# Kernel optimization log

Hardware: AMD Instinct MI355X
Metric: run time of the kernel (lower is better)

Reference implementation:

```python
import jax, jax.numpy as jnp
import numpy as np

E = 1280   # embed_dim
H = 16     # num_heads
D = E // H # head_dim = 80
S = 3072   # total tokens


def _rotate_half(x):
    x1, x2 = x[..., : D // 2], x[..., D // 2:]
    return jnp.concatenate((-x2, x1), axis=-1)


def setup_inputs() -> dict:
    key = jax.random.key(0)
    ks = jax.random.split(key, 7)
    x = jax.random.normal(ks[0], (S, E), dtype=jnp.float32)
    # rotary embeddings: cos/sin of random angles, shape (S, head_dim)
    ang = jax.random.uniform(ks[1], (S, D), dtype=jnp.float32) * (2 * np.pi)
    cos = jnp.cos(ang)
    sin = jnp.sin(ang)
    # 8 variable-length segments covering all S tokens
    cu_seqlens = jnp.array([0, 256, 640, 1024, 1536, 1920, 2304, 2688, 3072], dtype=jnp.int32)
    qkv_w = jax.random.normal(ks[2], (3 * E, E), dtype=jnp.float32) * 0.02
    qkv_b = jax.random.normal(ks[3], (3 * E,), dtype=jnp.float32) * 0.02
    proj_w = jax.random.normal(ks[4], (E, E), dtype=jnp.float32) * 0.02
    proj_b = jax.random.normal(ks[5], (E,), dtype=jnp.float32) * 0.02
    return {"x": x, "cu_seqlens": cu_seqlens, "cos": cos, "sin": sin,
            "qkv_w": qkv_w, "qkv_b": qkv_b, "proj_w": proj_w, "proj_b": proj_b}


def reference(x, cu_seqlens, cos, sin, qkv_w, qkv_b, proj_w, proj_b):
    # QKV projection: (S, 3E)
    qkv = x @ qkv_w.T + qkv_b
    q, k, v = jnp.split(qkv, 3, axis=-1)
    q = q.reshape(S, H, D)
    k = k.reshape(S, H, D)
    v = v.reshape(S, H, D)
    # inline RoPE, broadcast over heads (cos/sin: (S,1,D))
    c = cos[:, None, :]
    s = sin[:, None, :]
    q = q * c + _rotate_half(q) * s
    k = k * c + _rotate_half(k) * s
    # block-diagonal varlen attention: tokens attend only within their segment
    seg_ids = jnp.searchsorted(cu_seqlens, jnp.arange(S), side="right")  # (S,)
    mask = seg_ids[:, None] == seg_ids[None, :]                           # (S,S)
    scale = 1.0 / jnp.sqrt(jnp.asarray(D, dtype=q.dtype))
    scores = jnp.einsum("qhd,khd->hqk", q, k) * scale                    # (H,S,S)
    neg = jnp.finfo(scores.dtype).min
    scores = jnp.where(mask[None, :, :], scores, neg)
    attn = jax.nn.softmax(scores, axis=-1)
    out = jnp.einsum("hqk,khd->qhd", attn, v).reshape(S, E)
    return out @ proj_w.T + proj_b
```

## Files before the change

### kernel.cpp

```cpp
#include <hip/hip_runtime.h>
#include <hip/hip_bf16.h>

#define S_LEN 3072
#define E_DIM 1280
#define NH 16
#define HD 80
#define HDP 96
#define QKV_N 3840

typedef unsigned short u16;
typedef __bf16 bf16x8 __attribute__((ext_vector_type(8)));
typedef float f32x4 __attribute__((ext_vector_type(4)));

__device__ __forceinline__ u16 bf16_bits(float f) {
  __hip_bfloat16 b = __float2bfloat16(f);
  return *reinterpret_cast<u16*>(&b);
}
__device__ __forceinline__ float bf16_to_f(u16 u) {
  unsigned int x = ((unsigned int)u) << 16;
  return __uint_as_float(x);
}
__device__ __forceinline__ void gload_lds16(const u16* g, u16* l) {
  __builtin_amdgcn_global_load_lds(
      (const __attribute__((address_space(1))) void*)g,
      (__attribute__((address_space(3))) void*)l, 16, 0, 0);
}
__device__ __forceinline__ int imin(int a, int b) { return a < b ? a : b; }

#define XB_F4    983040
#define WQKV_F4  1228800
#define WPROJ_F4 409600
__global__ __launch_bounds__(256) void f32_to_bf16_3(const float* __restrict__ sx,
                                                     const float* __restrict__ sq,
                                                     const float* __restrict__ sp,
                                                     u16* __restrict__ dst) {
  int i = blockIdx.x * 256 + threadIdx.x;
  float4 v;
  if (i < XB_F4) v = reinterpret_cast<const float4*>(sx)[i];
  else if (i < XB_F4 + WQKV_F4) v = reinterpret_cast<const float4*>(sq)[i - XB_F4];
  else v = reinterpret_cast<const float4*>(sp)[i - XB_F4 - WQKV_F4];
  ushort4 o;
  o.x = bf16_bits(v.x); o.y = bf16_bits(v.y); o.z = bf16_bits(v.z); o.w = bf16_bits(v.w);
  reinterpret_cast<ushort4*>(dst)[i] = o;
}

template<int OUT_F32>
__global__ __launch_bounds__(256) void gemm_nt(const u16* __restrict__ A,
                                               const u16* __restrict__ B,
                                               const float* __restrict__ bias,
                                               void* __restrict__ Cout,
                                               int M, int N, int K, int nbx) {
  __shared__ u16 As[128 * 64];
  __shared__ u16 Bs[128 * 64];
  const int t = threadIdx.x;
  const int lane = t & 63;
  const int wave = t >> 6;
  const int l15 = lane & 15, l4 = lane >> 4;
  const int wm = (wave >> 1) * 64, wn = (wave & 1) * 64;

  const int nwg = gridDim.x;
  const int lg = (blockIdx.x & 7) * (nwg >> 3) + (blockIdx.x >> 3);
  const int m0 = (lg / nbx) * 128, n0 = (lg % nbx) * 128;

  const u16* gA[4];
  const u16* gB[4];
  u16* lA[4];
  u16* lB[4];
  #pragma unroll
  for (int i = 0; i < 4; ++i) {
    const int c = i * 256 + t;
    const int row = c >> 3;
    const int col = ((c & 7) ^ (row & 7)) * 8;
    gA[i] = A + (size_t)(m0 + row) * K + col;
    gB[i] = B + (size_t)(n0 + row) * K + col;
    lA[i] = &As[c * 8];
    lB[i] = &Bs[c * 8];
  }

  int aoff[4][2], boff[4][2];
  #pragma unroll
  for (int i = 0; i < 4; ++i)
    #pragma unroll
    for (int kk = 0; kk < 2; ++kk) {
      aoff[i][kk] = (wm + i * 16 + l15) * 64 + ((kk * 4 + l4) ^ (l15 & 7)) * 8;
      boff[i][kk] = (wn + i * 16 + l15) * 64 + ((kk * 4 + l4) ^ (l15 & 7)) * 8;
    }

  f32x4 acc[4][4] = {};

  const int nk = K >> 6;
  for (int kt = 0; kt < nk; ++kt) {
    const int k0 = kt << 6;
    #pragma unroll
    for (int i = 0; i < 4; ++i) gload_lds16(gA[i] + k0, lA[i]);
    #pragma unroll
    for (int i = 0; i < 4; ++i) gload_lds16(gB[i] + k0, lB[i]);
    __syncthreads();
    bf16x8 af[4][2], bfr[4][2];
    #pragma unroll
    for (int i = 0; i < 4; ++i)
      #pragma unroll
      for (int kk = 0; kk < 2; ++kk) {
        af[i][kk]  = *reinterpret_cast<const bf16x8*>(&As[aoff[i][kk]]);
        bfr[i][kk] = *reinterpret_cast<const bf16x8*>(&Bs[boff[i][kk]]);
      }
    __builtin_amdgcn_s_setprio(1);
    #pragma unroll
    for (int kk = 0; kk < 2; ++kk)
      #pragma unroll
      for (int i = 0; i < 4; ++i)
        #pragma unroll
        for (int j = 0; j < 4; ++j)
          acc[i][j] = __builtin_amdgcn_mfma_f32_16x16x32_bf16(af[i][kk], bfr[j][kk],
                                                              acc[i][j], 0, 0, 0);
    __builtin_amdgcn_s_setprio(0);
    __syncthreads();
  }

  #pragma unroll
  for (int i = 0; i < 4; ++i) {
    #pragma unroll
    for (int j = 0; j < 4; ++j) {
      const int col = n0 + wn + j * 16 + l15;
      const float bv = bias[col];
      const int rowb = m0 + wm + i * 16 + l4 * 4;
      #pragma unroll
      for (int r = 0; r < 4; ++r) {
        float v = acc[i][j][r] + bv;
        if (OUT_F32)
          reinterpret_cast<float*>(Cout)[(size_t)(rowb + r) * N + col] = v;
        else
          reinterpret_cast<u16*>(Cout)[(size_t)(rowb + r) * N + col] = bf16_bits(v);
      }
    }
  }
}

__global__ __launch_bounds__(256) void rope_scatter(const u16* __restrict__ qkv,
                                                    const float* __restrict__ cosb,
                                                    const float* __restrict__ sinb,
                                                    u16* __restrict__ qp,
                                                    u16* __restrict__ kp) {
  const int t = threadIdx.x;
  const int sl = t >> 6;
  const int p = t & 63;
  const int s = blockIdx.x * 4 + sl;
  const int h = blockIdx.y;
  const size_t ib = (size_t)s * QKV_N + h * HD;
  const size_t ob = ((size_t)h * S_LEN + s) * HDP;
  if (p < 40) {
    const float scale = 0.1118033988749895f;
    float q1 = bf16_to_f(qkv[ib + p]);
    float q2 = bf16_to_f(qkv[ib + 40 + p]);
    float k1 = bf16_to_f(qkv[ib + E_DIM + p]);
    float k2 = bf16_to_f(qkv[ib + E_DIM + 40 + p]);
    float c1 = cosb[(size_t)s * HD + p],      s1 = sinb[(size_t)s * HD + p];
    float c2 = cosb[(size_t)s * HD + 40 + p], s2 = sinb[(size_t)s * HD + 40 + p];
    qp[ob + p]      = bf16_bits((q1 * c1 - q2 * s1) * scale);
    qp[ob + 40 + p] = bf16_bits((q2 * c2 + q1 * s2) * scale);
    kp[ob + p]      = bf16_bits(k1 * c1 - k2 * s1);
    kp[ob + 40 + p] = bf16_bits(k2 * c2 + k1 * s2);
  } else if (p < 48) {
    const int pd = HD + (p - 40) * 2;
    qp[ob + pd] = 0; qp[ob + pd + 1] = 0;
    kp[ob + pd] = 0; kp[ob + pd + 1] = 0;
  }
}

__global__ __launch_bounds__(256) void v_transpose(const u16* __restrict__ qkv,
                                                   u16* __restrict__ vt) {
  const int idx = blockIdx.x * 256 + threadIdx.x;
  const int d = idx % HD;
  const int h = (idx / HD) % NH;
  const int sb = idx / (HD * NH);
  const int s0 = sb * 8;
  if (s0 >= S_LEN) return;
  u16 b[8];
  #pragma unroll
  for (int j = 0; j < 8; ++j)
    b[j] = qkv[(size_t)(s0 + j) * QKV_N + 2 * E_DIM + h * HD + d];
  uint4 pk;
  pk.x = b[0] | ((unsigned)b[1] << 16);
  pk.y = b[2] | ((unsigned)b[3] << 16);
  pk.z = b[4] | ((unsigned)b[5] << 16);
  pk.w = b[6] | ((unsigned)b[7] << 16);
  *reinterpret_cast<uint4*>(&vt[((size_t)h * HD + d) * S_LEN + s0]) = pk;
}

__global__ __launch_bounds__(256) void attn_fwd(const u16* __restrict__ qp,
                                                const u16* __restrict__ kp,
                                                const u16* __restrict__ vt,
                                                const int* __restrict__ cu, int ncu,
                                                u16* __restrict__ ao) {
  __shared__ u16 Ks[2][64][104];
  __shared__ u16 Pl[4][16][72];

  const int lg = ((blockIdx.x & 7) * 96) + (blockIdx.x >> 3);
  const int h = lg / 48;
  const int q0 = (lg % 48) * 64;

  const int t = threadIdx.x;
  const int wave = t >> 6;
  const int lane = t & 63;
  const int l15 = lane & 15, l4 = lane >> 4;
  const int qr = q0 + wave * 16;

  int lo = 0, hi = S_LEN;
  for (int i = 0; i + 1 < ncu; ++i) {
    int a = cu[i], b = cu[i + 1];
    if (q0 >= a && q0 < b) { lo = a; hi = b; }
  }
  const int nt = (hi - lo + 63) >> 6;

  const u16* qh = qp + (size_t)h * S_LEN * HDP;
  const u16* kh = kp + (size_t)h * S_LEN * HDP;
  const u16* vh = vt + (size_t)h * HD * S_LEN;

  bf16x8 qf[3];
  #pragma unroll
  for (int c = 0; c < 3; ++c)
    qf[c] = *reinterpret_cast<const bf16x8*>(&qh[(size_t)(qr + l15) * HDP + c * 32 + l4 * 8]);

  {
    bf16x8 kreg[3];
    #pragma unroll
    for (int i = 0; i < 3; ++i) {
      const int c2 = i * 256 + t;
      const int r = c2 / 12, cc = c2 % 12;
      const int row = imin(lo + r, S_LEN - 1);
      kreg[i] = *reinterpret_cast<const bf16x8*>(&kh[(size_t)row * HDP + cc * 8]);
    }
    #pragma unroll
    for (int i = 0; i < 3; ++i) {
      const int c2 = i * 256 + t;
      const int r = c2 / 12, cc = c2 % 12;
      *reinterpret_cast<bf16x8*>(&Ks[0][r][cc * 8]) = kreg[i];
    }
    __syncthreads();
  }

  f32x4 oacc[5] = {};
  float mrow[4], lrow[4];
  #pragma unroll
  for (int r = 0; r < 4; ++r) { mrow[r] = -INFINITY; lrow[r] = 0.f; }
  const float L2E = 1.4426950408889634f;

  int cur = 0;
  for (int ti = 0; ti < nt; ++ti) {
    const int kb = lo + ti * 64;
    const int kbL = imin(kb, S_LEN - 64);

    bf16x8 vreg[2][5];
    #pragma unroll
    for (int kc = 0; kc < 2; ++kc)
      #pragma unroll
      for (int df = 0; df < 5; ++df)
        vreg[kc][df] = *reinterpret_cast<const bf16x8*>(
            &vh[(size_t)(df * 16 + l15) * S_LEN + kbL + kc * 32 + l4 * 8]);

    const bool more = (ti + 1) < nt;
    bf16x8 kreg[3];
    if (more) {
      const int kb2 = lo + (ti + 1) * 64;
      #pragma unroll
      for (int i = 0; i < 3; ++i) {
        const int c2 = i * 256 + t;
        const int r = c2 / 12, cc = c2 % 12;
        const int row = imin(kb2 + r, S_LEN - 1);
        kreg[i] = *reinterpret_cast<const bf16x8*>(&kh[(size_t)row * HDP + cc * 8]);
      }
    }

    f32x4 sc[4];
    #pragma unroll
    for (int f = 0; f < 4; ++f) {
      f32x4 z = {0.f, 0.f, 0.f, 0.f};
      sc[f] = z;
    }
    __builtin_amdgcn_s_setprio(1);
    #pragma unroll
    for (int f = 0; f < 4; ++f)
      #pragma unroll
      for (int c = 0; c < 3; ++c) {
        bf16x8 kf = *reinterpret_cast<const bf16x8*>(&Ks[cur][f * 16 + l15][c * 32 + l4 * 8]);
        sc[f] = __builtin_amdgcn_mfma_f32_16x16x32_bf16(qf[c], kf, sc[f], 0, 0, 0);
      }
    __builtin_amdgcn_s_setprio(0);

    float scv[4][4], tm[4];
    #pragma unroll
    for (int r = 0; r < 4; ++r) tm[r] = -INFINITY;
    #pragma unroll
    for (int f = 0; f < 4; ++f) {
      const bool valid = (kb + f * 16 + l15) < hi;
      #pragma unroll
      for (int r = 0; r < 4; ++r) {
        float v = valid ? sc[f][r] : -INFINITY;
        scv[f][r] = v;
        tm[r] = fmaxf(tm[r], v);
      }
    }
    #pragma unroll
    for (int off = 1; off < 16; off <<= 1)
      #pragma unroll
      for (int r = 0; r < 4; ++r)
        tm[r] = fmaxf(tm[r], __shfl_xor(tm[r], off, 64));
    float corr[4], rs[4];
    #pragma unroll
    for (int r = 0; r < 4; ++r) {
      float mn = fmaxf(mrow[r], tm[r]);
      corr[r] = exp2f((mrow[r] - mn) * L2E);
      mrow[r] = mn;
      rs[r] = 0.f;
    }
    #pragma unroll
    for (int f = 0; f < 4; ++f)
      #pragma unroll
      for (int r = 0; r < 4; ++r) {
        float p = exp2f((scv[f][r] - mrow[r]) * L2E);
        rs[r] += p;
        Pl[wave][l4 * 4 + r][f * 16 + l15] = bf16_bits(p);
      }
    #pragma unroll
    for (int off = 1; off < 16; off <<= 1)
      #pragma unroll
      for (int r = 0; r < 4; ++r)
        rs[r] += __shfl_xor(rs[r], off, 64);
    #pragma unroll
    for (int r = 0; r < 4; ++r)
      lrow[r] = lrow[r] * corr[r] + rs[r];
    #pragma unroll
    for (int df = 0; df < 5; ++df)
      #pragma unroll
      for (int r = 0; r < 4; ++r)
        oacc[df][r] *= corr[r];
    asm volatile("s_waitcnt lgkmcnt(0)" ::: "memory");

    __builtin_amdgcn_s_setprio(1);
    #pragma unroll
    for (int kc = 0; kc < 2; ++kc) {
      bf16x8 pf = *reinterpret_cast<const bf16x8*>(&Pl[wave][l15][kc * 32 + l4 * 8]);
      #pragma unroll
      for (int df = 0; df < 5; ++df)
        oacc[df] = __builtin_amdgcn_mfma_f32_16x16x32_bf16(pf, vreg[kc][df], oacc[df], 0, 0, 0);
    }
    __builtin_amdgcn_s_setprio(0);

    if (more) {
      #pragma unroll
      for (int i = 0; i < 3; ++i) {
        const int c2 = i * 256 + t;
        const int r = c2 / 12, cc = c2 % 12;
        *reinterpret_cast<bf16x8*>(&Ks[cur ^ 1][r][cc * 8]) = kreg[i];
      }
    }
    __syncthreads();
    cur ^= 1;
  }

  #pragma unroll
  for (int df = 0; df < 5; ++df)
    #pragma unroll
    for (int r = 0; r < 4; ++r) {
      float v = oacc[df][r] / lrow[r];
      ao[(size_t)(qr + l4 * 4 + r) * E_DIM + h * HD + df * 16 + l15] = bf16_bits(v);
    }
}

extern "C" void kernel_launch(void* const* d_in, const int* in_sizes, int n_in,
                              void* d_out, int out_size, void* d_ws, size_t ws_size,
                              hipStream_t stream) {
  const float* x      = (const float*)d_in[0];
  const int*   cu     = (const int*)d_in[1];
  const float* cosb   = (const float*)d_in[2];
  const float* sinb   = (const float*)d_in[3];
  const float* qkv_w  = (const float*)d_in[4];
  const float* qkv_b  = (const float*)d_in[5];
  const float* proj_w = (const float*)d_in[6];
  const float* proj_b = (const float*)d_in[7];
  float* out = (float*)d_out;

  u16* xb     = (u16*)d_ws;
  u16* wqkvb  = xb     + (size_t)S_LEN * E_DIM;
  u16* wprojb = wqkvb  + (size_t)3 * E_DIM * E_DIM;
  u16* qkv    = wprojb + (size_t)E_DIM * E_DIM;
  u16* qp     = qkv    + (size_t)S_LEN * QKV_N;
  u16* kp     = qp     + (size_t)NH * S_LEN * HDP;
  u16* vt     = kp     + (size_t)NH * S_LEN * HDP;
  u16* attn   = vt     + (size_t)NH * HD * S_LEN;

  const int nf4 = XB_F4 + WQKV_F4 + WPROJ_F4;
  f32_to_bf16_3<<<nf4 / 256, 256, 0, stream>>>(x, qkv_w, proj_w, xb);

  gemm_nt<0><<<(QKV_N / 128) * (S_LEN / 128), 256, 0, stream>>>(
      xb, wqkvb, qkv_b, qkv, S_LEN, QKV_N, E_DIM, QKV_N / 128);

  rope_scatter<<<dim3(S_LEN / 4, NH), 256, 0, stream>>>(qkv, cosb, sinb, qp, kp);
  v_transpose<<<(NH * HD * (S_LEN / 8)) / 256, 256, 0, stream>>>(qkv, vt);

  attn_fwd<<<NH * (S_LEN / 64), 256, 0, stream>>>(qp, kp, vt, cu, in_sizes[1], attn);

  gemm_nt<1><<<(E_DIM / 128) * (S_LEN / 128), 256, 0, stream>>>(
      attn, wprojb, proj_b, out, S_LEN, E_DIM, E_DIM, E_DIM / 128);
}
```

Baseline: 127.4 us.

## Transpose attention MFMA operands so each lane owns one query row; lazy rescale

Swaps the A/B operands of both MFMAs so the score and output tiles come out transposed. Each lane then holds a single query row, which makes the running max and sum per-lane scalars and cuts the row reductions from 16-lane butterflies to two shuffles. It also adds a lazy rescale that only updates the max when it grows by more than 8, skips masking on full tiles, writes P with a swizzled 8-byte LDS layout, and stores the output as vectorized ushort4. The lazy threshold lets unnormalized probabilities grow up to about e^8 before rescaling, which trades some numerical headroom for fewer exp and multiply operations.

```diff
diff --git a/kernel.cpp b/kernel.cpp
--- a/kernel.cpp
+++ b/kernel.cpp
@@ -9,6 +9,7 @@
 #define QKV_N 3840
 
 typedef unsigned short u16;
+typedef unsigned int u32;
 typedef __bf16 bf16x8 __attribute__((ext_vector_type(8)));
 typedef float f32x4 __attribute__((ext_vector_type(4)));
 
@@ -240,10 +241,17 @@
   }
 
   f32x4 oacc[5] = {};
-  float mrow[4], lrow[4];
-  #pragma unroll
-  for (int r = 0; r < 4; ++r) { mrow[r] = -INFINITY; lrow[r] = 0.f; }
+  float mrow = -INFINITY, lrow = 0.f;
   const float L2E = 1.4426950408889634f;
+
+  int pwr[4];
+  #pragma unroll
+  for (int f = 0; f < 4; ++f)
+    pwr[f] = ((f * 2 + (l4 >> 1)) ^ (l15 & 7)) * 8 + (l4 & 1) * 4;
+  int prd[2];
+  #pragma unroll
+  for (int kc = 0; kc < 2; ++kc)
+    prd[kc] = ((kc * 4 + l4) ^ (l15 & 7)) * 8;
 
   int cur = 0;
   for (int ti = 0; ti < nt; ++ti) {
@@ -273,76 +281,70 @@
 
     f32x4 sc[4];
     #pragma unroll
-    for (int f = 0; f < 4; ++f) {
-      f32x4 z = {0.f, 0.f, 0.f, 0.f};
-      sc[f] = z;
-    }
+    for (int f = 0; f < 4; ++f) { f32x4 z = {0.f, 0.f, 0.f, 0.f}; sc[f] = z; }
     __builtin_amdgcn_s_setprio(1);
     #pragma unroll
     for (int f = 0; f < 4; ++f)
       #pragma unroll
       for (int c = 0; c < 3; ++c) {
         bf16x8 kf = *reinterpret_cast<const bf16x8*>(&Ks[cur][f * 16 + l15][c * 32 + l4 * 8]);
-        sc[f] = __builtin_amdgcn_mfma_f32_16x16x32_bf16(qf[c], kf, sc[f], 0, 0, 0);
+        sc[f] = __builtin_amdgcn_mfma_f32_16x16x32_bf16(kf, qf[c], sc[f], 0, 0, 0);
       }
     __builtin_amdgcn_s_setprio(0);
 
-    float scv[4][4], tm[4];
-    #pragma unroll
-    for (int r = 0; r < 4; ++r) tm[r] = -INFINITY;
+    if (kb + 64 > hi) {
+      #pragma unroll
+      for (int f = 0; f < 4; ++f)
+        #pragma unroll
+        for (int r = 0; r < 4; ++r)
+          if (kb + f * 16 + l4 * 4 + r >= hi) sc[f][r] = -INFINITY;
+    }
+
+    float tm = -INFINITY;
+    #pragma unroll
+    for (int f = 0; f < 4; ++f)
+      #pragma unroll
+      for (int r = 0; r < 4; ++r) tm = fmaxf(tm, sc[f][r]);
+    tm = fmaxf(tm, __shfl_xor(tm, 16, 64));
+    tm = fmaxf(tm, __shfl_xor(tm, 32, 64));
+
+    if (__any(tm > mrow + 8.f)) {
+      float mn = fmaxf(mrow, tm);
+      float corr = exp2f((mrow - mn) * L2E);
+      mrow = mn;
+      lrow *= corr;
+      #pragma unroll
+      for (int df = 0; df < 5; ++df)
+        #pragma unroll
+        for (int r = 0; r < 4; ++r) oacc[df][r] *= corr;
+    }
+
+    float rs = 0.f;
     #pragma unroll
     for (int f = 0; f < 4; ++f) {
-      const bool valid = (kb + f * 16 + l15) < hi;
-      #pragma unroll
-      for (int r = 0; r < 4; ++r) {
-        float v = valid ? sc[f][r] : -INFINITY;
-        scv[f][r] = v;
-        tm[r] = fmaxf(tm[r], v);
-      }
-    }
-    #pragma unroll
-    for (int off = 1; off < 16; off <<= 1)
-      #pragma unroll
-      for (int r = 0; r < 4; ++r)
-        tm[r] = fmaxf(tm[r], __shfl_xor(tm[r], off, 64));
-    float corr[4], rs[4];
-    #pragma unroll
-    for (int r = 0; r < 4; ++r) {
-      float mn = fmaxf(mrow[r], tm[r]);
-      corr[r] = exp2f((mrow[r] - mn) * L2E);
-      mrow[r] = mn;
-      rs[r] = 0.f;
-    }
-    #pragma unroll
-    for (int f = 0; f < 4; ++f)
-      #pragma unroll
-      for (int r = 0; r < 4; ++r) {
-        float p = exp2f((scv[f][r] - mrow[r]) * L2E);
-        rs[r] += p;
-        Pl[wave][l4 * 4 + r][f * 16 + l15] = bf16_bits(p);
-      }
-    #pragma unroll
-    for (int off = 1; off < 16; off <<= 1)
-      #pragma unroll
-      for (int r = 0; r < 4; ++r)
-        rs[r] += __shfl_xor(rs[r], off, 64);
-    #pragma unroll
-    for (int r = 0; r < 4; ++r)
-      lrow[r] = lrow[r] * corr[r] + rs[r];
-    #pragma unroll
-    for (int df = 0; df < 5; ++df)
-      #pragma unroll
-      for (int r = 0; r < 4; ++r)
-        oacc[df][r] *= corr[r];
+      float p0 = exp2f((sc[f][0] - mrow) * L2E);
+      float p1 = exp2f((sc[f][1] - mrow) * L2E);
+      float p2 = exp2f((sc[f][2] - mrow) * L2E);
+      float p3 = exp2f((sc[f][3] - mrow) * L2E);
+      rs += (p0 + p1) + (p2 + p3);
+      uint2 w;
+      w.x = (u32)bf16_bits(p0) | ((u32)bf16_bits(p1) << 16);
+      w.y = (u32)bf16_bits(p2) | ((u32)bf16_bits(p3) << 16);
+      *reinterpret_cast<uint2*>(&Pl[wave][l15][pwr[f]]) = w;
+    }
+    rs += __shfl_xor(rs, 16, 64);
+    rs += __shfl_xor(rs, 32, 64);
+    lrow += rs;
+
     asm volatile("s_waitcnt lgkmcnt(0)" ::: "memory");
 
     __builtin_amdgcn_s_setprio(1);
     #pragma unroll
     for (int kc = 0; kc < 2; ++kc) {
-      bf16x8 pf = *reinterpret_cast<const bf16x8*>(&Pl[wave][l15][kc * 32 + l4 * 8]);
+      bf16x8 pf = *reinterpret_cast<const bf16x8*>(&Pl[wave][l15][prd[kc]]);
       #pragma unroll
       for (int df = 0; df < 5; ++df)
-        oacc[df] = __builtin_amdgcn_mfma_f32_16x16x32_bf16(pf, vreg[kc][df], oacc[df], 0, 0, 0);
+        oacc[df] = __builtin_amdgcn_mfma_f32_16x16x32_bf16(vreg[kc][df], pf, oacc[df], 0, 0, 0);
     }
     __builtin_amdgcn_s_setprio(0);
 
@@ -358,13 +360,17 @@
     cur ^= 1;
   }
 
-  #pragma unroll
-  for (int df = 0; df < 5; ++df)
-    #pragma unroll
-    for (int r = 0; r < 4; ++r) {
-      float v = oacc[df][r] / lrow[r];
-      ao[(size_t)(qr + l4 * 4 + r) * E_DIM + h * HD + df * 16 + l15] = bf16_bits(v);
-    }
+  const float inv = 1.0f / lrow;
+  #pragma unroll
+  for (int df = 0; df < 5; ++df) {
+    ushort4 o;
+    o.x = bf16_bits(oacc[df][0] * inv);
+    o.y = bf16_bits(oacc[df][1] * inv);
+    o.z = bf16_bits(oacc[df][2] * inv);
+    o.w = bf16_bits(oacc[df][3] * inv);
+    *reinterpret_cast<ushort4*>(
+        &ao[(size_t)(qr + l15) * E_DIM + h * HD + df * 16 + l4 * 4]) = o;
+  }
 }
 
 extern "C" void kernel_launch(void* const* d_in, const int* in_sizes, int n_in,
```

After: 122.2 us. -4.1%, faster.
